# Performance work log

Hardware: AMD Instinct MI355X
Metric: run time of the kernel (lower is better)

The kernel has to match this reference:

```python
import jax, jax.numpy as jnp
import numpy as np

SIG_LEVEL = 2
UNIT = 128
SEQ = 64
BATCH = 256
SIG_DIM = UNIT + UNIT ** 2  # truncated signature dim for level 2
LN_EPS = 1e-5


def _signature(path, level):
    """Truncated path signature up to `level` via Chen's relation.
    path: (B, T, d) -> (B, d + d^2 + ... + d^level).
    Each segment contributes exp(dx): level-m term dx^{outer m}/m!.
    """
    B, T, d = path.shape
    dx = path[:, 1:] - path[:, :-1]  # (B, T-1, d)
    init = [jnp.zeros((B, d ** k), dtype=path.dtype) for k in range(1, level + 1)]

    def step(S, dxt):  # S: list of (B, d^k); dxt: (B, d)
        # P[m] = dxt^{outer m} / m!, flattened (B, d^m)
        P = [jnp.ones((B, 1), dtype=dxt.dtype), dxt]
        for m in range(2, level + 1):
            P.append((P[-1][:, :, None] * dxt[:, None, :]).reshape(B, d ** m) / m)
        newS = []
        for k in range(1, level + 1):
            s = P[k]  # j = 0 term (S_0 = 1)
            for j in range(1, k + 1):
                s = s + (S[j - 1][:, :, None] * P[k - j][:, None, :]).reshape(B, d ** k)
            newS.append(s)
        return newS, None

    S, _ = jax.lax.scan(step, init, jnp.swapaxes(dx, 0, 1))
    return jnp.concatenate(S, axis=-1)


def _grn_softmax(sig, W2, b2, W1, b1, Wg, bg, Wv, bv, Ws, bs, gamma, beta):
    # TFT-style gated residual network with softmax output activation.
    h = jax.nn.elu(sig @ W2 + b2)          # (B, unit)
    h = h @ W1 + b1                        # (B, unit)
    glu = jax.nn.sigmoid(h @ Wg + bg) * (h @ Wv + bv)
    skip = sig @ Ws + bs                   # residual projection sig_dim -> unit
    y = skip + glu
    mu = jnp.mean(y, axis=-1, keepdims=True)
    var = jnp.var(y, axis=-1, keepdims=True)
    y = (y - mu) * jax.lax.rsqrt(var + LN_EPS) * gamma + beta
    return jax.nn.softmax(y, axis=-1)


def setup_inputs() -> dict:
    key = jax.random.key(0)
    ks = jax.random.split(key, 16)
    s = 0.02
    return {
        "inputs": jax.random.normal(ks[0], (BATCH, SEQ, UNIT), dtype=jnp.float32),
        "time_kernel": jnp.ones((SEQ, 1), dtype=jnp.float32),
        "Wd": jax.random.normal(ks[1], (UNIT, UNIT), dtype=jnp.float32) * s,
        "bd": jnp.zeros((UNIT,), dtype=jnp.float32),
        "W2": jax.random.normal(ks[2], (SIG_DIM, UNIT), dtype=jnp.float32) * s,
        "b2": jnp.zeros((UNIT,), dtype=jnp.float32),
        "W1": jax.random.normal(ks[3], (UNIT, UNIT), dtype=jnp.float32) * s,
        "b1": jnp.zeros((UNIT,), dtype=jnp.float32),
        "Wg": jax.random.normal(ks[4], (UNIT, UNIT), dtype=jnp.float32) * s,
        "bg": jnp.zeros((UNIT,), dtype=jnp.float32),
        "Wv": jax.random.normal(ks[5], (UNIT, UNIT), dtype=jnp.float32) * s,
        "bv": jnp.zeros((UNIT,), dtype=jnp.float32),
        "Ws": jax.random.normal(ks[6], (SIG_DIM, UNIT), dtype=jnp.float32) * s,
        "bs": jnp.zeros((UNIT,), dtype=jnp.float32),
        "gamma": jnp.ones((UNIT,), dtype=jnp.float32),
        "beta": jnp.zeros((UNIT,), dtype=jnp.float32),
    }


def reference(inputs, time_kernel, Wd, bd, W2, b2, W1, b1, Wg, bg, Wv, bv, Ws, bs, gamma, beta):
    x = time_kernel * inputs                         # (B, T, d) time weighting
    sig = _signature(x, SIG_LEVEL)                   # (B, sig_dim)
    weights = _grn_softmax(sig, W2, b2, W1, b1, Wg, bg, Wv, bv, Ws, bs, gamma, beta)  # (B, d)
    dense_out = x @ Wd + bd                          # (B, T, d); dropout is identity at eval
    return dense_out * weights[:, None, :]
```

## Files before the change

kernel.cpp:

```cpp
#include <hip/hip_runtime.h>
#include <math.h>

#define SD 16512
#define NCH 32
#define RPSTRIDE 8192
#define LN_EPS 1e-5f

typedef __attribute__((ext_vector_type(4))) float f32x4;
typedef __attribute__((ext_vector_type(8))) short bf16x8;

__device__ __forceinline__ unsigned bfpack(float lo, float hi) {
    unsigned a = __builtin_bit_cast(unsigned, lo);
    unsigned b = __builtin_bit_cast(unsigned, hi);
    a = (a + 0x7FFFu + ((a >> 16) & 1u)) >> 16;
    b = (b + 0x7FFFu + ((b >> 16) & 1u)) >> 16;
    return a | (b << 16);
}
__device__ __forceinline__ unsigned short bf1(float x) {
    unsigned a = __builtin_bit_cast(unsigned, x);
    return (unsigned short)((a + 0x7FFFu + ((a >> 16) & 1u)) >> 16);
}

__global__ __launch_bounds__(512) void k_sig(const float* __restrict__ x,
                                             const float* __restrict__ tk,
                                             const float* __restrict__ Wd,
                                             unsigned short* __restrict__ sig,
                                             unsigned short* __restrict__ xbf,
                                             unsigned short* __restrict__ WdTg) {
    __shared__ unsigned short Ut[128][72];
    __shared__ unsigned short DXt[128][72];
    __shared__ float tks[64];
    int tid = threadIdx.x;
    int b = blockIdx.x;

    if (b == 256) {
        int d = tid & 127, kh = tid >> 7;
        unsigned* dst = (unsigned*)WdTg;
        for (int kk = 0; kk < 32; kk += 2) {
            int k = kh * 32 + kk;
            float v0 = Wd[(size_t)k * 128 + d];
            float v1 = Wd[(size_t)(k + 1) * 128 + d];
            dst[d * 64 + (k >> 1)] = bfpack(v0, v1);
        }
        return;
    }

    if (tid < 64) tks[tid] = tk[tid];
    __syncthreads();

    const float* xb = x + (size_t)b * 8192;
    unsigned short* xbb = xbf + (size_t)b * 8192;
    int i = tid & 127, th = tid >> 7;

    float x0 = tks[0] * xb[i];
    float xa = tks[th * 16] * xb[(size_t)(th * 16) * 128 + i];
    #pragma unroll
    for (int tp = 0; tp < 8; ++tp) {
        int p = th * 8 + tp;
        int t0 = 2 * p;
        float xv = tks[t0 + 1] * xb[(size_t)(t0 + 1) * 128 + i];
        float dx0 = xv - xa, u0 = 0.5f * (xa + xv) - x0;
        float dx1, u1, xc;
        if (p == 31) { dx1 = 0.f; u1 = 0.f; xc = 0.f; }
        else {
            xc = tks[t0 + 2] * xb[(size_t)(t0 + 2) * 128 + i];
            dx1 = xc - xv; u1 = 0.5f * (xv + xc) - x0;
        }
        *(unsigned*)&Ut[i][t0]  = bfpack(u0, u1);
        *(unsigned*)&DXt[i][t0] = bfpack(dx0, dx1);
        xbb[(size_t)t0 * 128 + i]       = bf1(xa);
        xbb[(size_t)(t0 + 1) * 128 + i] = bf1(xv);
        if (p == 31) sig[(size_t)b * SD + i] = bf1(xv - x0);
        xa = xc;
    }
    __syncthreads();

    int w = tid >> 6, lane = tid & 63;
    int wm = w >> 2, wn = w & 3;
    int l15 = lane & 15, lg = lane >> 4;
    f32x4 acc[4][2];
    #pragma unroll
    for (int m = 0; m < 4; ++m)
        #pragma unroll
        for (int n = 0; n < 2; ++n) acc[m][n] = (f32x4){0.f, 0.f, 0.f, 0.f};

    #pragma unroll
    for (int ks = 0; ks < 2; ++ks) {
        bf16x8 af[4], bfv[2];
        #pragma unroll
        for (int m = 0; m < 4; ++m)
            af[m] = *(const bf16x8*)&Ut[wm * 64 + m * 16 + l15][ks * 32 + lg * 8];
        #pragma unroll
        for (int n = 0; n < 2; ++n)
            bfv[n] = *(const bf16x8*)&DXt[wn * 32 + n * 16 + l15][ks * 32 + lg * 8];
        #pragma unroll
        for (int m = 0; m < 4; ++m)
            #pragma unroll
            for (int n = 0; n < 2; ++n)
                acc[m][n] = __builtin_amdgcn_mfma_f32_16x16x32_bf16(af[m], bfv[n], acc[m][n], 0, 0, 0);
    }

    unsigned short* sp = sig + (size_t)b * SD + 128;
    #pragma unroll
    for (int m = 0; m < 4; ++m)
        #pragma unroll
        for (int n = 0; n < 2; ++n)
            #pragma unroll
            for (int rr = 0; rr < 4; ++rr)
                sp[(size_t)(wm * 64 + m * 16 + lg * 4 + rr) * 128 + wn * 32 + n * 16 + l15]
                    = bf1(acc[m][n][rr]);
}

__global__ __launch_bounds__(512, 2) void k_gemm(const unsigned short* __restrict__ sig,
                                                 const float* __restrict__ W2,
                                                 const float* __restrict__ Ws,
                                                 unsigned* __restrict__ partial_p) {
    __shared__ unsigned short As[128 * 128];
    __shared__ unsigned short Bs[32 * 128];

    int p = blockIdx.x;
    int lid = (p & 7) * 64 + (p >> 3);
    int ch = lid >> 4;
    int mt = (lid >> 3) & 1;
    int nt = lid & 7;
    const float* W = (nt < 4) ? W2 : Ws;
    int ntc = (nt & 3) * 32;
    int kb0 = ch * 512;
    int nsub = (ch == 31) ? 5 : 4;

    int tid = threadIdx.x;
    int w = tid >> 6, lane = tid & 63;
    int l15 = lane & 15, lg = lane >> 4;
    const unsigned short* sigB = sig + (size_t)(mt * 128) * SD;

    int arow = tid >> 2;
    int aq   = (tid & 3) * 32;
    int bk   = tid >> 2;
    int bc0  = (tid & 3) * 8;

    f32x4 acc[2];
    acc[0] = (f32x4){0.f, 0.f, 0.f, 0.f};
    acc[1] = (f32x4){0.f, 0.f, 0.f, 0.f};

    for (int s = 0; s < nsub; ++s) {
        int kb = kb0 + s * 128;
        {
            const unsigned short* src = sigB + (size_t)arow * SD + kb + aq;
            int sw = (arow & 7) << 3;
            #pragma unroll
            for (int j = 0; j < 4; ++j) {
                uint4 v = *(const uint4*)(src + j * 8);
                *(uint4*)&As[arow * 128 + ((aq + j * 8) ^ sw)] = v;
            }
        }
        {
            const float* wp = W + (size_t)(kb + bk) * 128 + ntc + bc0;
            f32x4 t0 = *(const f32x4*)wp;
            f32x4 t1 = *(const f32x4*)(wp + 4);
            float v[8] = {t0[0], t0[1], t0[2], t0[3], t1[0], t1[1], t1[2], t1[3]};
            #pragma unroll
            for (int u = 0; u < 8; ++u) {
                int c = bc0 + u;
                Bs[c * 128 + (bk ^ ((c & 7) << 3))] = bf1(v[u]);
            }
        }
        __syncthreads();

        #pragma unroll
        for (int ks = 0; ks < 4; ++ks) {
            int ko = ks * 32 + lg * 8;
            bf16x8 af, bfv[2];
            {
                int row = w * 16 + l15;
                af = *(const bf16x8*)&As[row * 128 + (ko ^ ((row & 7) << 3))];
            }
            #pragma unroll
            for (int n = 0; n < 2; ++n) {
                int col = n * 16 + l15;
                bfv[n] = *(const bf16x8*)&Bs[col * 128 + (ko ^ ((col & 7) << 3))];
            }
            acc[0] = __builtin_amdgcn_mfma_f32_16x16x32_bf16(af, bfv[0], acc[0], 0, 0, 0);
            acc[1] = __builtin_amdgcn_mfma_f32_16x16x32_bf16(af, bfv[1], acc[1], 0, 0, 0);
        }
        __syncthreads();
    }

    int r0 = mt * 128 + w * 16 + lg * 4;
    int rp0 = r0 >> 1;
    #pragma unroll
    for (int n = 0; n < 2; ++n) {
        int colg = nt * 32 + n * 16 + l15;
        partial_p[(size_t)rp0 * RPSTRIDE + ch * 256 + colg]
            = bfpack(acc[n][0], acc[n][1]);
        partial_p[(size_t)(rp0 + 1) * RPSTRIDE + ch * 256 + colg]
            = bfpack(acc[n][2], acc[n][3]);
    }
}

__global__ __launch_bounds__(512) void k_tail(const unsigned* __restrict__ partial_p,
                                              const unsigned short* __restrict__ xbf,
                                              const unsigned short* __restrict__ WdTg,
                                              const float* __restrict__ b2,
                                              const float* __restrict__ W1,
                                              const float* __restrict__ b1,
                                              const float* __restrict__ Wg,
                                              const float* __restrict__ bg,
                                              const float* __restrict__ Wv,
                                              const float* __restrict__ bv,
                                              const float* __restrict__ bs,
                                              const float* __restrict__ gamma,
                                              const float* __restrict__ beta,
                                              const float* __restrict__ bd,
                                              float* __restrict__ out) {
    __shared__ float hs[128], ss[128], h2s[128];
    __shared__ float red4[4][128], rtmp[2][256];
    __shared__ float ys[128], es[128], wts[128];

    int b = blockIdx.x, tid = threadIdx.x;
    int lane = tid & 63;
    int l15 = lane & 15, lg = lane >> 4;

    {
        int c = tid & 255, h = tid >> 8;
        float s = 0.f;
        const unsigned* Pp = partial_p + (size_t)(b >> 1) * RPSTRIDE + c;
        bool hi = (b & 1) != 0;
        #pragma unroll 8
        for (int ch = h; ch < NCH; ch += 2) {
            unsigned u = Pp[ch * 256];
            unsigned hw = hi ? (u & 0xffff0000u) : (u << 16);
            s += __builtin_bit_cast(float, hw);
        }
        rtmp[h][c] = s;
    }
    __syncthreads();
    if (tid < 256) {
        float rsum = rtmp[0][tid] + rtmp[1][tid];
        if (tid < 128) {
            float hp = rsum + b2[tid];
            hs[tid] = hp > 0.f ? hp : expm1f(hp);
        } else {
            ss[tid - 128] = rsum + bs[tid - 128];
        }
    }
    __syncthreads();

    int c = tid & 127;
    {
        int qt = tid >> 7;
        float s = 0.f;
        int kbq = qt * 32;
        #pragma unroll 8
        for (int k = 0; k < 32; ++k) s += hs[kbq + k] * W1[(size_t)(kbq + k) * 128 + c];
        red4[qt][c] = s;
    }
    __syncthreads();
    if (tid < 128)
        h2s[tid] = red4[0][tid] + red4[1][tid] + red4[2][tid] + red4[3][tid] + b1[tid];
    __syncthreads();
    {
        int idx = tid >> 7, sel = idx & 1, kh = idx >> 1;
        const float* Wx = sel ? Wv : Wg;
        float s = 0.f;
        int kbq = kh * 64;
        #pragma unroll 8
        for (int k = 0; k < 64; ++k) s += h2s[kbq + k] * Wx[(size_t)(kbq + k) * 128 + c];
        red4[idx][c] = s;
    }
    __syncthreads();
    if (tid < 128) {
        float g = 1.f / (1.f + expf(-(red4[0][c] + red4[2][c] + bg[c])));
        float v = red4[1][c] + red4[3][c] + bv[c];
        ys[c] = ss[c] + g * v;
    }
    __syncthreads();
    if (tid < 128) {
        float sum = 0.f, sq = 0.f;
        for (int k = 0; k < 128; ++k) { float v = ys[k]; sum += v; sq += v * v; }
        float mu = sum * (1.f / 128.f);
        float var = sq * (1.f / 128.f) - mu * mu;
        float rs = rsqrtf(var + LN_EPS);
        es[c] = (ys[c] - mu) * rs * gamma[c] + beta[c];
    }
    __syncthreads();
    if (tid < 128) {
        float m = -1e30f;
        for (int k = 0; k < 128; ++k) m = fmaxf(m, es[k]);
        ys[c] = expf(es[c] - m);
    }
    __syncthreads();
    if (tid < 128) {
        float se = 0.f;
        for (int k = 0; k < 128; ++k) se += ys[k];
        wts[c] = ys[c] / se;
    }
    __syncthreads();

    int w4 = tid >> 6;
    const unsigned short* xrow = xbf + (size_t)b * 8192;
    f32x4 dacc[4];
    #pragma unroll
    for (int fm = 0; fm < 4; ++fm) dacc[fm] = (f32x4){0.f, 0.f, 0.f, 0.f};
    #pragma unroll
    for (int ks = 0; ks < 4; ++ks) {
        bf16x8 av[4], bv2;
        #pragma unroll
        for (int fm = 0; fm < 4; ++fm)
            av[fm] = *(const bf16x8*)(xrow + (size_t)(fm * 16 + l15) * 128 + ks * 32 + lg * 8);
        bv2 = *(const bf16x8*)(WdTg + (size_t)(w4 * 16 + l15) * 128 + ks * 32 + lg * 8);
        #pragma unroll
        for (int fm = 0; fm < 4; ++fm)
            dacc[fm] = __builtin_amdgcn_mfma_f32_16x16x32_bf16(av[fm], bv2, dacc[fm], 0, 0, 0);
    }
    int dcol = w4 * 16 + l15;
    float bdv = bd[dcol], wtv = wts[dcol];
    #pragma unroll
    for (int fm = 0; fm < 4; ++fm)
        #pragma unroll
        for (int rr = 0; rr < 4; ++rr) {
            int t = fm * 16 + lg * 4 + rr;
            out[(size_t)b * 8192 + (size_t)t * 128 + dcol] = (dacc[fm][rr] + bdv) * wtv;
        }
}

extern "C" void kernel_launch(void* const* d_in, const int* in_sizes, int n_in,
                              void* d_out, int out_size, void* d_ws, size_t ws_size,
                              hipStream_t stream) {
    const float* inputs = (const float*)d_in[0];
    const float* tk     = (const float*)d_in[1];
    const float* Wd     = (const float*)d_in[2];
    const float* bd     = (const float*)d_in[3];
    const float* W2     = (const float*)d_in[4];
    const float* b2     = (const float*)d_in[5];
    const float* W1     = (const float*)d_in[6];
    const float* b1     = (const float*)d_in[7];
    const float* Wg     = (const float*)d_in[8];
    const float* bg     = (const float*)d_in[9];
    const float* Wv     = (const float*)d_in[10];
    const float* bv     = (const float*)d_in[11];
    const float* Wsk    = (const float*)d_in[12];
    const float* bs     = (const float*)d_in[13];
    const float* gamma  = (const float*)d_in[14];
    const float* beta   = (const float*)d_in[15];
    float* out = (float*)d_out;

    char* ws = (char*)d_ws;
    unsigned short* sig  = (unsigned short*)ws;
    unsigned* partial_p  = (unsigned*)(ws + 8454144);
    unsigned short* xbf  = (unsigned short*)(ws + 12648448);
    unsigned short* WdTg = (unsigned short*)(ws + 16842752);

    k_sig <<<257, 512, 0, stream>>>(inputs, tk, Wd, sig, xbf, WdTg);
    k_gemm<<<512, 512, 0, stream>>>(sig, W2, Wsk, partial_p);
    k_tail<<<256, 512, 0, stream>>>(partial_p, xbf, WdTg, b2, W1, b1, Wg, bg, Wv, bv,
                                    bs, gamma, beta, bd, out);
}
```

Measured before the change: 40.24 us.

## Register double-buffer global loads in sig GEMM and use shuffle reductions in tail

The sig-projection GEMM now prefetches the next K-slice of A and W into registers while the current slice is staged into LDS and computed. The W load pattern changes so each thread reads two consecutive K rows and packs them into a single 32-bit bf16 pair store. The tail kernel's LayerNorm and softmax reductions switch from serial 128-element LDS loops to wavefront shuffle reductions. These changes aim to hide global load latency and cut the serial reduction work, at the cost of extra registers.

```diff
diff --git a/kernel.cpp b/kernel.cpp
--- a/kernel.cpp
+++ b/kernel.cpp
@@ -135,55 +135,69 @@
 
     int arow = tid >> 2;
     int aq   = (tid & 3) * 32;
-    int bk   = tid >> 2;
-    int bc0  = (tid & 3) * 8;
+    int asw  = (arow & 7) << 3;
+    int kpr  = (lane) * 2;
+    int bc4  = w * 4;
 
     f32x4 acc[2];
     acc[0] = (f32x4){0.f, 0.f, 0.f, 0.f};
     acc[1] = (f32x4){0.f, 0.f, 0.f, 0.f};
 
-    for (int s = 0; s < nsub; ++s) {
-        int kb = kb0 + s * 128;
-        {
-            const unsigned short* src = sigB + (size_t)arow * SD + kb + aq;
-            int sw = (arow & 7) << 3;
-            #pragma unroll
-            for (int j = 0; j < 4; ++j) {
-                uint4 v = *(const uint4*)(src + j * 8);
-                *(uint4*)&As[arow * 128 + ((aq + j * 8) ^ sw)] = v;
-            }
-        }
-        {
-            const float* wp = W + (size_t)(kb + bk) * 128 + ntc + bc0;
-            f32x4 t0 = *(const f32x4*)wp;
-            f32x4 t1 = *(const f32x4*)(wp + 4);
-            float v[8] = {t0[0], t0[1], t0[2], t0[3], t1[0], t1[1], t1[2], t1[3]};
-            #pragma unroll
-            for (int u = 0; u < 8; ++u) {
-                int c = bc0 + u;
-                Bs[c * 128 + (bk ^ ((c & 7) << 3))] = bf1(v[u]);
-            }
-        }
-        __syncthreads();
-
-        #pragma unroll
-        for (int ks = 0; ks < 4; ++ks) {
-            int ko = ks * 32 + lg * 8;
-            bf16x8 af, bfv[2];
-            {
-                int row = w * 16 + l15;
-                af = *(const bf16x8*)&As[row * 128 + (ko ^ ((row & 7) << 3))];
-            }
-            #pragma unroll
-            for (int n = 0; n < 2; ++n) {
-                int col = n * 16 + l15;
-                bfv[n] = *(const bf16x8*)&Bs[col * 128 + (ko ^ ((col & 7) << 3))];
-            }
-            acc[0] = __builtin_amdgcn_mfma_f32_16x16x32_bf16(af, bfv[0], acc[0], 0, 0, 0);
-            acc[1] = __builtin_amdgcn_mfma_f32_16x16x32_bf16(af, bfv[1], acc[1], 0, 0, 0);
-        }
-        __syncthreads();
-    }
+    uint4 aR0[4], aR1[4];
+    f32x4 bR0[2], bR1[2];
+
+#define LOADG(AR, BR, s)                                                           \
+    {                                                                              \
+        int kb = kb0 + (s) * 128;                                                  \
+        const unsigned short* asrc = sigB + (size_t)arow * SD + kb + aq;           \
+        _Pragma("unroll")                                                          \
+        for (int j = 0; j < 4; ++j) AR[j] = *(const uint4*)(asrc + j * 8);         \
+        const float* wp = W + (size_t)(kb + kpr) * 128 + ntc + bc4;                \
+        BR[0] = *(const f32x4*)wp;                                                 \
+        BR[1] = *(const f32x4*)(wp + 128);                                         \
+    }
+
+#define STAGE_COMPUTE(AR, BR)                                                      \
+    {                                                                              \
+        _Pragma("unroll")                                                          \
+        for (int j = 0; j < 4; ++j)                                                \
+            *(uint4*)&As[arow * 128 + ((aq + j * 8) ^ asw)] = AR[j];               \
+        _Pragma("unroll")                                                          \
+        for (int u = 0; u < 4; ++u) {                                              \
+            int c = bc4 + u;                                                       \
+            *(unsigned*)&Bs[c * 128 + (kpr ^ ((c & 7) << 3))]                      \
+                = bfpack(BR[0][u], BR[1][u]);                                      \
+        }                                                                          \
+        __syncthreads();                                                           \
+        _Pragma("unroll")                                                          \
+        for (int ks = 0; ks < 4; ++ks) {                                           \
+            int ko = ks * 32 + lg * 8;                                             \
+            int row = w * 16 + l15;                                                \
+            bf16x8 af = *(const bf16x8*)&As[row * 128 + (ko ^ ((row & 7) << 3))];  \
+            bf16x8 bf0, bf1v;                                                      \
+            { int col = l15;      bf0  = *(const bf16x8*)&Bs[col * 128 + (ko ^ ((col & 7) << 3))]; } \
+            { int col = 16 + l15; bf1v = *(const bf16x8*)&Bs[col * 128 + (ko ^ ((col & 7) << 3))]; } \
+            acc[0] = __builtin_amdgcn_mfma_f32_16x16x32_bf16(af, bf0,  acc[0], 0, 0, 0); \
+            acc[1] = __builtin_amdgcn_mfma_f32_16x16x32_bf16(af, bf1v, acc[1], 0, 0, 0); \
+        }                                                                          \
+        __syncthreads();                                                           \
+    }
+
+    LOADG(aR0, bR0, 0);
+    int s = 0;
+    while (true) {
+        bool more1 = (s + 1 < nsub);
+        if (more1) LOADG(aR1, bR1, s + 1);
+        STAGE_COMPUTE(aR0, bR0);
+        if (!more1) break;
+        bool more2 = (s + 2 < nsub);
+        if (more2) LOADG(aR0, bR0, s + 2);
+        STAGE_COMPUTE(aR1, bR1);
+        if (!more2) break;
+        s += 2;
+    }
+#undef LOADG
+#undef STAGE_COMPUTE
 
     int r0 = mt * 128 + w * 16 + lg * 4;
     int rp0 = r0 >> 1;
@@ -214,7 +228,8 @@
                                               float* __restrict__ out) {
     __shared__ float hs[128], ss[128], h2s[128];
     __shared__ float red4[4][128], rtmp[2][256];
-    __shared__ float ys[128], es[128], wts[128];
+    __shared__ float ys[128], wts[128];
+    __shared__ float wred[2][4];
 
     int b = blockIdx.x, tid = threadIdx.x;
     int lane = tid & 63;
@@ -268,31 +283,46 @@
         red4[idx][c] = s;
     }
     __syncthreads();
+
+    float yv = 0.f, yn = 0.f, e = 0.f;
     if (tid < 128) {
         float g = 1.f / (1.f + expf(-(red4[0][c] + red4[2][c] + bg[c])));
         float v = red4[1][c] + red4[3][c] + bv[c];
-        ys[c] = ss[c] + g * v;
+        yv = ss[c] + g * v;
+        float s1 = yv, s2 = yv * yv;
+        #pragma unroll
+        for (int off = 1; off < 64; off <<= 1) {
+            s1 += __shfl_xor(s1, off, 64);
+            s2 += __shfl_xor(s2, off, 64);
+        }
+        if (lane == 0) { wred[0][tid >> 6] = s1; wred[1][tid >> 6] = s2; }
     }
     __syncthreads();
     if (tid < 128) {
-        float sum = 0.f, sq = 0.f;
-        for (int k = 0; k < 128; ++k) { float v = ys[k]; sum += v; sq += v * v; }
+        float sum = wred[0][0] + wred[0][1];
+        float sq  = wred[1][0] + wred[1][1];
         float mu = sum * (1.f / 128.f);
         float var = sq * (1.f / 128.f) - mu * mu;
         float rs = rsqrtf(var + LN_EPS);
-        es[c] = (ys[c] - mu) * rs * gamma[c] + beta[c];
+        yn = (yv - mu) * rs * gamma[c] + beta[c];
+        float m = yn;
+        #pragma unroll
+        for (int off = 1; off < 64; off <<= 1) m = fmaxf(m, __shfl_xor(m, off, 64));
+        if (lane == 0) wred[0][tid >> 6] = m;
     }
     __syncthreads();
     if (tid < 128) {
-        float m = -1e30f;
-        for (int k = 0; k < 128; ++k) m = fmaxf(m, es[k]);
-        ys[c] = expf(es[c] - m);
+        float m = fmaxf(wred[0][0], wred[0][1]);
+        e = expf(yn - m);
+        float s = e;
+        #pragma unroll
+        for (int off = 1; off < 64; off <<= 1) s += __shfl_xor(s, off, 64);
+        if (lane == 0) wred[1][tid >> 6] = s;
     }
     __syncthreads();
     if (tid < 128) {
-        float se = 0.f;
-        for (int k = 0; k < 128; ++k) se += ys[k];
-        wts[c] = ys[c] / se;
+        float se = wred[1][0] + wred[1][1];
+        wts[c] = e / se;
     }
     __syncthreads();
 
```

Measured after the change: 60.30 us. +49.9%, slower.
